# Kernel optimization log

Hardware: AMD Instinct MI355X
Metric: run time of the kernel (lower is better)

The kernel has to match this reference:

```python
import jax, jax.numpy as jnp
import numpy as np

B, IN_DIM, HID, ATT = 16384, 128, 512, 256
TOTAL = IN_DIM + HID + ATT


def setup_inputs() -> dict:
    key = jax.random.key(0)
    ks = jax.random.split(key, 10)
    u = lambda k, shape, lo, hi: jax.random.uniform(k, shape, jnp.float32, lo, hi)
    return {
        "t": jnp.float32(0.0),
        "h_ltc": jax.random.normal(ks[0], (B, HID), jnp.float32),
        "x_t": jax.random.normal(ks[1], (B, IN_DIM), jnp.float32),
        "context": jax.random.normal(ks[2], (B, ATT), jnp.float32),
        "W_gd": u(ks[3], (2 * HID, TOTAL), -0.1, 0.1),
        "b_gd": u(ks[4], (2 * HID,), -0.1, 0.1),
        "W_tau": u(ks[5], (HID, HID), -0.1, 0.1),
        "b_tau": u(ks[6], (HID,), -0.1, 0.1),
        "gleak": u(ks[7], (HID,), 0.001, 1.0),
        "cm": u(ks[8], (HID,), 0.4, 0.6),
    }


def reference(t, h_ltc, x_t, context, W_gd, b_gd, W_tau, b_tau, gleak, cm):
    # combined: [B, IN+HID+ATT]
    combined = jnp.concatenate([x_t, h_ltc, context], axis=1)
    g_d = combined @ W_gd.T + b_gd            # [B, 2*HID]
    gate, dynamics = jnp.split(g_d, 2, axis=1)
    tau = jax.nn.softplus(h_ltc @ W_tau.T + b_tau)  # [B, HID]
    numerator = jax.nn.sigmoid(gate) * jnp.tanh(dynamics) - h_ltc
    denominator = tau + jax.nn.softplus(cm) + jax.nn.softplus(gleak)
    return numerator / (denominator + 1e-6)
```

## Files before the change

kernel.cpp:

```cpp
#include <hip/hip_runtime.h>
#include <hip/hip_bf16.h>
#include <math.h>

#define BROWS 16384
#define IN_DIM 128
#define HID 512
#define ATT 256
#define KTOT 896
#define KC_TOT 112

typedef __bf16 bf16x8 __attribute__((ext_vector_type(8)));
typedef float f32x4 __attribute__((ext_vector_type(4)));

__device__ __forceinline__ float softplus_f(float x) {
    return fmaxf(x, 0.0f) + log1pf(__expf(-fabsf(x)));
}

__global__ void pack_B(const float* __restrict__ W_gd, const float* __restrict__ W_tau,
                       const float* __restrict__ gleak, const float* __restrict__ cm,
                       __hip_bfloat16* __restrict__ B_stage, float* __restrict__ dconst) {
    const int cid = blockIdx.x * 256 + threadIdx.x;
    if (cid < HID) {
        dconst[cid] = softplus_f(cm[cid]) + softplus_f(gleak[cid]) + 1e-6f;
    }
    const int nl = cid % 192;
    const int kc = (cid / 192) % KC_TOT;
    const int jt = cid / (192 * KC_TOT);
    const int jg = nl / 48, type = (nl % 48) / 16, j16 = nl % 16;
    const int j = jt * 64 + jg * 16 + j16;
    const int k0 = kc * 8;

    float v[8];
    if (type == 0) {
        const float* s = W_gd + (size_t)j * KTOT + k0;
        #pragma unroll
        for (int i = 0; i < 8; ++i) v[i] = s[i];
    } else if (type == 1) {
        const float* s = W_gd + (size_t)(HID + j) * KTOT + k0;
        #pragma unroll
        for (int i = 0; i < 8; ++i) v[i] = s[i];
    } else {
        if (k0 >= IN_DIM && k0 < IN_DIM + HID) {
            const float* s = W_tau + (size_t)j * HID + (k0 - IN_DIM);
            #pragma unroll
            for (int i = 0; i < 8; ++i) v[i] = s[i];
        } else {
            #pragma unroll
            for (int i = 0; i < 8; ++i) v[i] = 0.0f;
        }
    }
    union { __hip_bfloat16 hh[8]; uint4 u; } p;
    #pragma unroll
    for (int i = 0; i < 8; ++i) p.hh[i] = __float2bfloat16(v[i]);
    *(uint4*)(B_stage + (size_t)cid * 8) = p.u;
}

__device__ __forceinline__ void slab_src(int ks, const float* x, const float* h,
                                         const float* c, const float*& src,
                                         int& rs, int& c0) {
    if (ks < 2)       { src = x; rs = IN_DIM; c0 = ks * 64; }
    else if (ks < 10) { src = h; rs = HID;    c0 = (ks - 2) * 64; }
    else              { src = c; rs = ATT;    c0 = (ks - 10) * 64; }
}

__global__ __launch_bounds__(512, 4) void ltc_gemm(
    const float* __restrict__ x, const float* __restrict__ h_ltc,
    const float* __restrict__ ctx, const __hip_bfloat16* __restrict__ B_stage,
    const float* __restrict__ b_gd, const float* __restrict__ b_tau,
    const float* __restrict__ dconst, float* __restrict__ out) {

    __shared__ __attribute__((aligned(16))) char smem[16384 + 24576];
    char* As = smem;
    char* Bs = smem + 16384;

    const int bx = blockIdx.x;
    const int mt = bx & 127;
    const int jt = bx >> 7;
    const int tid = threadIdx.x;
    const int wave = tid >> 6, lane = tid & 63;
    const int wm = wave >> 2;
    const int wj = wave & 3;
    const int q = lane >> 4, t = lane & 15;

    const int kc8 = tid & 7;
    const int mi0 = tid >> 3;

    f32x4 accg[4], accd[4], acct[4];
    #pragma unroll
    for (int i = 0; i < 4; ++i) {
        accg[i] = (f32x4)0.0f; accd[i] = (f32x4)0.0f; acct[i] = (f32x4)0.0f;
    }

    const __hip_bfloat16* bSrc[3]; char* bDst[3];
    #pragma unroll
    for (int r = 0; r < 3; ++r) {
        int c = wave + 8 * r;
        bSrc[r] = B_stage + (size_t)jt * (KC_TOT * 1536) + c * 512 + lane * 8;
        bDst[r] = Bs + c * 1024;
    }

    float4 pf[2][2];
    {
        const float* src; int rs, c0;
        slab_src(0, x, h_ltc, ctx, src, rs, c0);
        #pragma unroll
        for (int r = 0; r < 2; ++r) {
            const float* p = src + (size_t)(mt * 128 + mi0 + 64 * r) * rs + c0 + kc8 * 8;
            pf[r][0] = *(const float4*)p;
            pf[r][1] = *(const float4*)(p + 4);
        }
    }

    for (int ks = 0; ks < 14; ++ks) {
        #pragma unroll
        for (int r = 0; r < 3; ++r)
            __builtin_amdgcn_global_load_lds(
                (const __attribute__((address_space(1))) void*)bSrc[r],
                (__attribute__((address_space(3))) void*)bDst[r], 16, 0, 0);
        #pragma unroll
        for (int r = 0; r < 2; ++r) {
            union { __hip_bfloat16 hh[8]; uint4 u; } pk;
            pk.hh[0] = __float2bfloat16(pf[r][0].x);
            pk.hh[1] = __float2bfloat16(pf[r][0].y);
            pk.hh[2] = __float2bfloat16(pf[r][0].z);
            pk.hh[3] = __float2bfloat16(pf[r][0].w);
            pk.hh[4] = __float2bfloat16(pf[r][1].x);
            pk.hh[5] = __float2bfloat16(pf[r][1].y);
            pk.hh[6] = __float2bfloat16(pf[r][1].z);
            pk.hh[7] = __float2bfloat16(pf[r][1].w);
            const int mi = mi0 + 64 * r;
            *(uint4*)(As + ((kc8 * 128 + (mi ^ kc8)) << 4)) = pk.u;
        }
        __syncthreads();

        if (ks < 13) {
            const float* src; int rs, c0;
            slab_src(ks + 1, x, h_ltc, ctx, src, rs, c0);
            #pragma unroll
            for (int r = 0; r < 2; ++r) {
                const float* p = src + (size_t)(mt * 128 + mi0 + 64 * r) * rs + c0 + kc8 * 8;
                pf[r][0] = *(const float4*)p;
                pf[r][1] = *(const float4*)(p + 4);
            }
        }

        const bool tau_on = (ks >= 2 && ks < 10);
        #pragma unroll
        for (int ko2 = 0; ko2 < 2; ++ko2) {
            const int kcl = ko2 * 4 + q;
            const char* ab = As + ((kcl * 128 + ((wm * 64 + t) ^ kcl)) << 4);
            bf16x8 a0 = *(const bf16x8*)(ab);
            bf16x8 a1 = *(const bf16x8*)(ab + 256);
            bf16x8 a2 = *(const bf16x8*)(ab + 512);
            bf16x8 a3 = *(const bf16x8*)(ab + 768);
            const char* bb = Bs + (((kcl * 192) + wj * 48 + t) << 4);
            bf16x8 bg = *(const bf16x8*)(bb);
            bf16x8 bd = *(const bf16x8*)(bb + 256);
            accg[0] = __builtin_amdgcn_mfma_f32_16x16x32_bf16(a0, bg, accg[0], 0, 0, 0);
            accg[1] = __builtin_amdgcn_mfma_f32_16x16x32_bf16(a1, bg, accg[1], 0, 0, 0);
            accg[2] = __builtin_amdgcn_mfma_f32_16x16x32_bf16(a2, bg, accg[2], 0, 0, 0);
            accg[3] = __builtin_amdgcn_mfma_f32_16x16x32_bf16(a3, bg, accg[3], 0, 0, 0);
            accd[0] = __builtin_amdgcn_mfma_f32_16x16x32_bf16(a0, bd, accd[0], 0, 0, 0);
            accd[1] = __builtin_amdgcn_mfma_f32_16x16x32_bf16(a1, bd, accd[1], 0, 0, 0);
            accd[2] = __builtin_amdgcn_mfma_f32_16x16x32_bf16(a2, bd, accd[2], 0, 0, 0);
            accd[3] = __builtin_amdgcn_mfma_f32_16x16x32_bf16(a3, bd, accd[3], 0, 0, 0);
            if (tau_on) {
                bf16x8 bt = *(const bf16x8*)(bb + 512);
                acct[0] = __builtin_amdgcn_mfma_f32_16x16x32_bf16(a0, bt, acct[0], 0, 0, 0);
                acct[1] = __builtin_amdgcn_mfma_f32_16x16x32_bf16(a1, bt, acct[1], 0, 0, 0);
                acct[2] = __builtin_amdgcn_mfma_f32_16x16x32_bf16(a2, bt, acct[2], 0, 0, 0);
                acct[3] = __builtin_amdgcn_mfma_f32_16x16x32_bf16(a3, bt, acct[3], 0, 0, 0);
            }
        }
        #pragma unroll
        for (int r = 0; r < 3; ++r) bSrc[r] += 12288;
        __syncthreads();
    }

    const int row0 = mt * 128 + wm * 64 + q * 4;
    const int j = jt * 64 + wj * 16 + t;
    const float bgj = b_gd[j];
    const float bdj = b_gd[HID + j];
    const float btj = b_tau[j];
    const float dcj = dconst[j];
    #pragma unroll
    for (int i = 0; i < 4; ++i) {
        #pragma unroll
        for (int r = 0; r < 4; ++r) {
            const int row = row0 + i * 16 + r;
            const float gv = accg[i][r] + bgj;
            const float dv = accd[i][r] + bdj;
            const float tp = acct[i][r] + btj;
            const float hv = h_ltc[(size_t)row * HID + j];
            const float sig = __builtin_amdgcn_rcpf(1.0f + __expf(-gv));
            const float th  = 1.0f - 2.0f * __builtin_amdgcn_rcpf(__expf(2.0f * dv) + 1.0f);
            const float tau = fmaxf(tp, 0.0f) + __logf(1.0f + __expf(-fabsf(tp)));
            out[(size_t)row * HID + j] = (sig * th - hv) * __builtin_amdgcn_rcpf(tau + dcj);
        }
    }
}

extern "C" void kernel_launch(void* const* d_in, const int* in_sizes, int n_in,
                              void* d_out, int out_size, void* d_ws, size_t ws_size,
                              hipStream_t stream) {
    const float* h_ltc = (const float*)d_in[1];
    const float* x_t   = (const float*)d_in[2];
    const float* ctx   = (const float*)d_in[3];
    const float* W_gd  = (const float*)d_in[4];
    const float* b_gd  = (const float*)d_in[5];
    const float* W_tau = (const float*)d_in[6];
    const float* b_tau = (const float*)d_in[7];
    const float* gleak = (const float*)d_in[8];
    const float* cm    = (const float*)d_in[9];

    char* ws = (char*)d_ws;
    __hip_bfloat16* B_stage = (__hip_bfloat16*)ws;
    float* dconst = (float*)(ws + 2752512);

    pack_B<<<672, 256, 0, stream>>>(W_gd, W_tau, gleak, cm, B_stage, dconst);
    ltc_gemm<<<1024, 512, 0, stream>>>(x_t, h_ltc, ctx, B_stage, b_gd, b_tau, dconst,
                                       (float*)d_out);
}
```

Baseline: 169.0 us.

## Halve output-column tile and double-buffer A/B LDS stages

Shrinks each block's output tile from 64 to 32 hidden columns, which doubles the grid to 2048 blocks. The eight waves are rearranged as a 4x2 grid, each holding a 32x16 sub-tile. A and B LDS buffers are now double-buffered with a two-deep register prefetch of activations, so the next slab's conversion and async B load overlap the current MFMA work and one barrier per step goes away. In exchange, activations are re-read from global memory twice as often and LDS use grows, which may lower occupancy.

Result: slower. 203.9 us (+20.6%).

```diff
diff --git a/kernel.cpp b/kernel.cpp
--- a/kernel.cpp
+++ b/kernel.cpp
@@ -23,11 +23,11 @@
     if (cid < HID) {
         dconst[cid] = softplus_f(cm[cid]) + softplus_f(gleak[cid]) + 1e-6f;
     }
-    const int nl = cid % 192;
-    const int kc = (cid / 192) % KC_TOT;
-    const int jt = cid / (192 * KC_TOT);
+    const int nl = cid % 96;
+    const int kc = (cid / 96) % KC_TOT;
+    const int jt = cid / (96 * KC_TOT);
     const int jg = nl / 48, type = (nl % 48) / 16, j16 = nl % 16;
-    const int j = jt * 64 + jg * 16 + j16;
+    const int j = jt * 32 + jg * 16 + j16;
     const int k0 = kc * 8;
 
     float v[8];
@@ -69,78 +69,121 @@
     const float* __restrict__ b_gd, const float* __restrict__ b_tau,
     const float* __restrict__ dconst, float* __restrict__ out) {
 
-    __shared__ __attribute__((aligned(16))) char smem[16384 + 24576];
-    char* As = smem;
-    char* Bs = smem + 16384;
+    __shared__ __attribute__((aligned(16))) char smem[2 * 16384 + 2 * 12288];
 
     const int bx = blockIdx.x;
     const int mt = bx & 127;
     const int jt = bx >> 7;
     const int tid = threadIdx.x;
     const int wave = tid >> 6, lane = tid & 63;
-    const int wm = wave >> 2;
-    const int wj = wave & 3;
+    const int wm = wave >> 1;
+    const int wj = wave & 1;
     const int q = lane >> 4, t = lane & 15;
 
     const int kc8 = tid & 7;
     const int mi0 = tid >> 3;
 
-    f32x4 accg[4], accd[4], acct[4];
+    f32x4 accg[2], accd[2], acct[2];
     #pragma unroll
-    for (int i = 0; i < 4; ++i) {
+    for (int i = 0; i < 2; ++i) {
         accg[i] = (f32x4)0.0f; accd[i] = (f32x4)0.0f; acct[i] = (f32x4)0.0f;
     }
 
-    const __hip_bfloat16* bSrc[3]; char* bDst[3];
-    #pragma unroll
-    for (int r = 0; r < 3; ++r) {
-        int c = wave + 8 * r;
-        bSrc[r] = B_stage + (size_t)jt * (KC_TOT * 1536) + c * 512 + lane * 8;
-        bDst[r] = Bs + c * 1024;
-    }
-
-    float4 pf[2][2];
+    const __hip_bfloat16* bSrc0 = B_stage + (size_t)jt * (KC_TOT * 768)
+                                + wave * 512 + lane * 8;
+    const __hip_bfloat16* bSrc1 = bSrc0 + 8 * 512;
+
+    float4 pf[2][2][2];
     {
         const float* src; int rs, c0;
         slab_src(0, x, h_ltc, ctx, src, rs, c0);
         #pragma unroll
         for (int r = 0; r < 2; ++r) {
             const float* p = src + (size_t)(mt * 128 + mi0 + 64 * r) * rs + c0 + kc8 * 8;
-            pf[r][0] = *(const float4*)p;
-            pf[r][1] = *(const float4*)(p + 4);
-        }
-    }
-
-    for (int ks = 0; ks < 14; ++ks) {
-        #pragma unroll
-        for (int r = 0; r < 3; ++r)
-            __builtin_amdgcn_global_load_lds(
-                (const __attribute__((address_space(1))) void*)bSrc[r],
-                (__attribute__((address_space(3))) void*)bDst[r], 16, 0, 0);
+            pf[0][r][0] = *(const float4*)p;
+            pf[0][r][1] = *(const float4*)(p + 4);
+        }
+    }
+    {
+        char* As0 = smem;
         #pragma unroll
         for (int r = 0; r < 2; ++r) {
             union { __hip_bfloat16 hh[8]; uint4 u; } pk;
-            pk.hh[0] = __float2bfloat16(pf[r][0].x);
-            pk.hh[1] = __float2bfloat16(pf[r][0].y);
-            pk.hh[2] = __float2bfloat16(pf[r][0].z);
-            pk.hh[3] = __float2bfloat16(pf[r][0].w);
-            pk.hh[4] = __float2bfloat16(pf[r][1].x);
-            pk.hh[5] = __float2bfloat16(pf[r][1].y);
-            pk.hh[6] = __float2bfloat16(pf[r][1].z);
-            pk.hh[7] = __float2bfloat16(pf[r][1].w);
+            pk.hh[0] = __float2bfloat16(pf[0][r][0].x);
+            pk.hh[1] = __float2bfloat16(pf[0][r][0].y);
+            pk.hh[2] = __float2bfloat16(pf[0][r][0].z);
+            pk.hh[3] = __float2bfloat16(pf[0][r][0].w);
+            pk.hh[4] = __float2bfloat16(pf[0][r][1].x);
+            pk.hh[5] = __float2bfloat16(pf[0][r][1].y);
+            pk.hh[6] = __float2bfloat16(pf[0][r][1].z);
+            pk.hh[7] = __float2bfloat16(pf[0][r][1].w);
             const int mi = mi0 + 64 * r;
-            *(uint4*)(As + ((kc8 * 128 + (mi ^ kc8)) << 4)) = pk.u;
-        }
-        __syncthreads();
+            *(uint4*)(As0 + ((kc8 * 128 + (mi ^ kc8)) << 4)) = pk.u;
+        }
+        char* Bs0 = smem + 32768;
+        __builtin_amdgcn_global_load_lds(
+            (const __attribute__((address_space(1))) void*)bSrc0,
+            (__attribute__((address_space(3))) void*)(Bs0 + wave * 1024), 16, 0, 0);
+        if (wave < 4)
+            __builtin_amdgcn_global_load_lds(
+                (const __attribute__((address_space(1))) void*)bSrc1,
+                (__attribute__((address_space(3))) void*)(Bs0 + (wave + 8) * 1024), 16, 0, 0);
+    }
+    {
+        const float* src; int rs, c0;
+        slab_src(1, x, h_ltc, ctx, src, rs, c0);
+        #pragma unroll
+        for (int r = 0; r < 2; ++r) {
+            const float* p = src + (size_t)(mt * 128 + mi0 + 64 * r) * rs + c0 + kc8 * 8;
+            pf[1][r][0] = *(const float4*)p;
+            pf[1][r][1] = *(const float4*)(p + 4);
+        }
+    }
+    __syncthreads();
+
+    for (int ks = 0; ks < 14; ++ks) {
+        const int cur = ks & 1, nxt = cur ^ 1;
+        char* AsC = smem + cur * 16384;
+        char* AsN = smem + nxt * 16384;
+        char* BsC = smem + 32768 + cur * 12288;
+        char* BsN = smem + 32768 + nxt * 12288;
 
         if (ks < 13) {
+            const int slot = (ks + 1) & 1;
+            #pragma unroll
+            for (int r = 0; r < 2; ++r) {
+                union { __hip_bfloat16 hh[8]; uint4 u; } pk;
+                pk.hh[0] = __float2bfloat16(pf[slot][r][0].x);
+                pk.hh[1] = __float2bfloat16(pf[slot][r][0].y);
+                pk.hh[2] = __float2bfloat16(pf[slot][r][0].z);
+                pk.hh[3] = __float2bfloat16(pf[slot][r][0].w);
+                pk.hh[4] = __float2bfloat16(pf[slot][r][1].x);
+                pk.hh[5] = __float2bfloat16(pf[slot][r][1].y);
+                pk.hh[6] = __float2bfloat16(pf[slot][r][1].z);
+                pk.hh[7] = __float2bfloat16(pf[slot][r][1].w);
+                const int mi = mi0 + 64 * r;
+                *(uint4*)(AsN + ((kc8 * 128 + (mi ^ kc8)) << 4)) = pk.u;
+            }
+            const __hip_bfloat16* b0 = bSrc0 + (size_t)(ks + 1) * 6144;
+            __builtin_amdgcn_global_load_lds(
+                (const __attribute__((address_space(1))) void*)b0,
+                (__attribute__((address_space(3))) void*)(BsN + wave * 1024), 16, 0, 0);
+            if (wave < 4) {
+                const __hip_bfloat16* b1 = bSrc1 + (size_t)(ks + 1) * 6144;
+                __builtin_amdgcn_global_load_lds(
+                    (const __attribute__((address_space(1))) void*)b1,
+                    (__attribute__((address_space(3))) void*)(BsN + (wave + 8) * 1024), 16, 0, 0);
+            }
+        }
+        if (ks < 12) {
             const float* src; int rs, c0;
-            slab_src(ks + 1, x, h_ltc, ctx, src, rs, c0);
+            slab_src(ks + 2, x, h_ltc, ctx, src, rs, c0);
+            const int slot = ks & 1;
             #pragma unroll
             for (int r = 0; r < 2; ++r) {
                 const float* p = src + (size_t)(mt * 128 + mi0 + 64 * r) * rs + c0 + kc8 * 8;
-                pf[r][0] = *(const float4*)p;
-                pf[r][1] = *(const float4*)(p + 4);
+                pf[slot][r][0] = *(const float4*)p;
+                pf[slot][r][1] = *(const float4*)(p + 4);
             }
         }
 
@@ -148,43 +191,33 @@
         #pragma unroll
         for (int ko2 = 0; ko2 < 2; ++ko2) {
             const int kcl = ko2 * 4 + q;
-            const char* ab = As + ((kcl * 128 + ((wm * 64 + t) ^ kcl)) << 4);
+            const char* ab = AsC + ((kcl * 128 + wm * 32 + (t ^ kcl)) << 4);
             bf16x8 a0 = *(const bf16x8*)(ab);
             bf16x8 a1 = *(const bf16x8*)(ab + 256);
-            bf16x8 a2 = *(const bf16x8*)(ab + 512);
-            bf16x8 a3 = *(const bf16x8*)(ab + 768);
-            const char* bb = Bs + (((kcl * 192) + wj * 48 + t) << 4);
+            const char* bb = BsC + ((kcl * 96 + wj * 48 + t) << 4);
             bf16x8 bg = *(const bf16x8*)(bb);
             bf16x8 bd = *(const bf16x8*)(bb + 256);
             accg[0] = __builtin_amdgcn_mfma_f32_16x16x32_bf16(a0, bg, accg[0], 0, 0, 0);
             accg[1] = __builtin_amdgcn_mfma_f32_16x16x32_bf16(a1, bg, accg[1], 0, 0, 0);
-            accg[2] = __builtin_amdgcn_mfma_f32_16x16x32_bf16(a2, bg, accg[2], 0, 0, 0);
-            accg[3] = __builtin_amdgcn_mfma_f32_16x16x32_bf16(a3, bg, accg[3], 0, 0, 0);
             accd[0] = __builtin_amdgcn_mfma_f32_16x16x32_bf16(a0, bd, accd[0], 0, 0, 0);
             accd[1] = __builtin_amdgcn_mfma_f32_16x16x32_bf16(a1, bd, accd[1], 0, 0, 0);
-            accd[2] = __builtin_amdgcn_mfma_f32_16x16x32_bf16(a2, bd, accd[2], 0, 0, 0);
-            accd[3] = __builtin_amdgcn_mfma_f32_16x16x32_bf16(a3, bd, accd[3], 0, 0, 0);
             if (tau_on) {
                 bf16x8 bt = *(const bf16x8*)(bb + 512);
                 acct[0] = __builtin_amdgcn_mfma_f32_16x16x32_bf16(a0, bt, acct[0], 0, 0, 0);
                 acct[1] = __builtin_amdgcn_mfma_f32_16x16x32_bf16(a1, bt, acct[1], 0, 0, 0);
-                acct[2] = __builtin_amdgcn_mfma_f32_16x16x32_bf16(a2, bt, acct[2], 0, 0, 0);
-                acct[3] = __builtin_amdgcn_mfma_f32_16x16x32_bf16(a3, bt, acct[3], 0, 0, 0);
-            }
-        }
-        #pragma unroll
-        for (int r = 0; r < 3; ++r) bSrc[r] += 12288;
+            }
+        }
         __syncthreads();
     }
 
-    const int row0 = mt * 128 + wm * 64 + q * 4;
-    const int j = jt * 64 + wj * 16 + t;
+    const int row0 = mt * 128 + wm * 32 + q * 4;
+    const int j = jt * 32 + wj * 16 + t;
     const float bgj = b_gd[j];
     const float bdj = b_gd[HID + j];
     const float btj = b_tau[j];
     const float dcj = dconst[j];
     #pragma unroll
-    for (int i = 0; i < 4; ++i) {
+    for (int i = 0; i < 2; ++i) {
         #pragma unroll
         for (int r = 0; r < 4; ++r) {
             const int row = row0 + i * 16 + r;
@@ -218,6 +251,6 @@
     float* dconst = (float*)(ws + 2752512);
 
     pack_B<<<672, 256, 0, stream>>>(W_gd, W_tau, gleak, cm, B_stage, dconst);
-    ltc_gemm<<<1024, 512, 0, stream>>>(x_t, h_ltc, ctx, B_stage, b_gd, b_tau, dconst,
+    ltc_gemm<<<2048, 512, 0, stream>>>(x_t, h_ltc, ctx, B_stage, b_gd, b_tau, dconst,
                                        (float*)d_out);
 }
```

## Double-buffer A tile in LDS and load B fragments directly from global

Applied to the files above, without the earlier changes.

Replaces the single A buffer plus LDS-staged B with a ping-pong A buffer in LDS, so the next slab is written while the current one is consumed and only one barrier per k-step remains. B fragments are now read by each wave straight from global memory into registers instead of going through global_load_lds. The A prefetch distance grows to two slabs and the loop is fully unrolled. This removes a barrier and the LDS staging traffic for B, but each wave now issues redundant global reads of B that rely on cache hits, and register pressure rises.

Result: no change. 171.9 us (+1.7%).

```diff
diff --git a/kernel.cpp b/kernel.cpp
--- a/kernel.cpp
+++ b/kernel.cpp
@@ -69,9 +69,7 @@
     const float* __restrict__ b_gd, const float* __restrict__ b_tau,
     const float* __restrict__ dconst, float* __restrict__ out) {
 
-    __shared__ __attribute__((aligned(16))) char smem[16384 + 24576];
-    char* As = smem;
-    char* Bs = smem + 16384;
+    __shared__ __attribute__((aligned(16))) char smem[2 * 16384];
 
     const int bx = blockIdx.x;
     const int mt = bx & 127;
@@ -91,13 +89,8 @@
         accg[i] = (f32x4)0.0f; accd[i] = (f32x4)0.0f; acct[i] = (f32x4)0.0f;
     }
 
-    const __hip_bfloat16* bSrc[3]; char* bDst[3];
-    #pragma unroll
-    for (int r = 0; r < 3; ++r) {
-        int c = wave + 8 * r;
-        bSrc[r] = B_stage + (size_t)jt * (KC_TOT * 1536) + c * 512 + lane * 8;
-        bDst[r] = Bs + c * 1024;
-    }
+    const __hip_bfloat16* bBase = B_stage + (size_t)jt * (KC_TOT * 1536)
+                                + (size_t)(wj * 48 + t) * 8;
 
     float4 pf[2][2];
     {
@@ -110,13 +103,8 @@
             pf[r][1] = *(const float4*)(p + 4);
         }
     }
-
-    for (int ks = 0; ks < 14; ++ks) {
-        #pragma unroll
-        for (int r = 0; r < 3; ++r)
-            __builtin_amdgcn_global_load_lds(
-                (const __attribute__((address_space(1))) void*)bSrc[r],
-                (__attribute__((address_space(3))) void*)bDst[r], 16, 0, 0);
+    {
+        char* As0 = smem;
         #pragma unroll
         for (int r = 0; r < 2; ++r) {
             union { __hip_bfloat16 hh[8]; uint4 u; } pk;
@@ -129,13 +117,56 @@
             pk.hh[6] = __float2bfloat16(pf[r][1].z);
             pk.hh[7] = __float2bfloat16(pf[r][1].w);
             const int mi = mi0 + 64 * r;
-            *(uint4*)(As + ((kc8 * 128 + (mi ^ kc8)) << 4)) = pk.u;
-        }
-        __syncthreads();
+            *(uint4*)(As0 + ((kc8 * 128 + (mi ^ kc8)) << 4)) = pk.u;
+        }
+    }
+    {
+        const float* src; int rs, c0;
+        slab_src(1, x, h_ltc, ctx, src, rs, c0);
+        #pragma unroll
+        for (int r = 0; r < 2; ++r) {
+            const float* p = src + (size_t)(mt * 128 + mi0 + 64 * r) * rs + c0 + kc8 * 8;
+            pf[r][0] = *(const float4*)p;
+            pf[r][1] = *(const float4*)(p + 4);
+        }
+    }
+    __syncthreads();
+
+    #pragma unroll
+    for (int ks = 0; ks < 14; ++ks) {
+        char* AsC = smem + (ks & 1) * 16384;
+        char* AsN = smem + ((ks & 1) ^ 1) * 16384;
+        const bool tau_on = (ks >= 2 && ks < 10);
+
+        bf16x8 Bv[2][3];
+        #pragma unroll
+        for (int ko2 = 0; ko2 < 2; ++ko2) {
+            const int kcl = ko2 * 4 + q;
+            const __hip_bfloat16* bp = bBase + (size_t)(ks * 8 + kcl) * 1536;
+            Bv[ko2][0] = *(const bf16x8*)(bp);
+            Bv[ko2][1] = *(const bf16x8*)(bp + 128);
+            if (tau_on) Bv[ko2][2] = *(const bf16x8*)(bp + 256);
+        }
 
         if (ks < 13) {
+            #pragma unroll
+            for (int r = 0; r < 2; ++r) {
+                union { __hip_bfloat16 hh[8]; uint4 u; } pk;
+                pk.hh[0] = __float2bfloat16(pf[r][0].x);
+                pk.hh[1] = __float2bfloat16(pf[r][0].y);
+                pk.hh[2] = __float2bfloat16(pf[r][0].z);
+                pk.hh[3] = __float2bfloat16(pf[r][0].w);
+                pk.hh[4] = __float2bfloat16(pf[r][1].x);
+                pk.hh[5] = __float2bfloat16(pf[r][1].y);
+                pk.hh[6] = __float2bfloat16(pf[r][1].z);
+                pk.hh[7] = __float2bfloat16(pf[r][1].w);
+                const int mi = mi0 + 64 * r;
+                *(uint4*)(AsN + ((kc8 * 128 + (mi ^ kc8)) << 4)) = pk.u;
+            }
+        }
+        if (ks < 12) {
             const float* src; int rs, c0;
-            slab_src(ks + 1, x, h_ltc, ctx, src, rs, c0);
+            slab_src(ks + 2, x, h_ltc, ctx, src, rs, c0);
             #pragma unroll
             for (int r = 0; r < 2; ++r) {
                 const float* p = src + (size_t)(mt * 128 + mi0 + 64 * r) * rs + c0 + kc8 * 8;
@@ -144,36 +175,29 @@
             }
         }
 
-        const bool tau_on = (ks >= 2 && ks < 10);
         #pragma unroll
         for (int ko2 = 0; ko2 < 2; ++ko2) {
             const int kcl = ko2 * 4 + q;
-            const char* ab = As + ((kcl * 128 + ((wm * 64 + t) ^ kcl)) << 4);
+            const char* ab = AsC + ((kcl * 128 + ((wm * 64 + t) ^ kcl)) << 4);
             bf16x8 a0 = *(const bf16x8*)(ab);
             bf16x8 a1 = *(const bf16x8*)(ab + 256);
             bf16x8 a2 = *(const bf16x8*)(ab + 512);
             bf16x8 a3 = *(const bf16x8*)(ab + 768);
-            const char* bb = Bs + (((kcl * 192) + wj * 48 + t) << 4);
-            bf16x8 bg = *(const bf16x8*)(bb);
-            bf16x8 bd = *(const bf16x8*)(bb + 256);
-            accg[0] = __builtin_amdgcn_mfma_f32_16x16x32_bf16(a0, bg, accg[0], 0, 0, 0);
-            accg[1] = __builtin_amdgcn_mfma_f32_16x16x32_bf16(a1, bg, accg[1], 0, 0, 0);
-            accg[2] = __builtin_amdgcn_mfma_f32_16x16x32_bf16(a2, bg, accg[2], 0, 0, 0);
-            accg[3] = __builtin_amdgcn_mfma_f32_16x16x32_bf16(a3, bg, accg[3], 0, 0, 0);
-            accd[0] = __builtin_amdgcn_mfma_f32_16x16x32_bf16(a0, bd, accd[0], 0, 0, 0);
-            accd[1] = __builtin_amdgcn_mfma_f32_16x16x32_bf16(a1, bd, accd[1], 0, 0, 0);
-            accd[2] = __builtin_amdgcn_mfma_f32_16x16x32_bf16(a2, bd, accd[2], 0, 0, 0);
-            accd[3] = __builtin_amdgcn_mfma_f32_16x16x32_bf16(a3, bd, accd[3], 0, 0, 0);
+            accg[0] = __builtin_amdgcn_mfma_f32_16x16x32_bf16(a0, Bv[ko2][0], accg[0], 0, 0, 0);
+            accg[1] = __builtin_amdgcn_mfma_f32_16x16x32_bf16(a1, Bv[ko2][0], accg[1], 0, 0, 0);
+            accg[2] = __builtin_amdgcn_mfma_f32_16x16x32_bf16(a2, Bv[ko2][0], accg[2], 0, 0, 0);
+            accg[3] = __builtin_amdgcn_mfma_f32_16x16x32_bf16(a3, Bv[ko2][0], accg[3], 0, 0, 0);
+            accd[0] = __builtin_amdgcn_mfma_f32_16x16x32_bf16(a0, Bv[ko2][1], accd[0], 0, 0, 0);
+            accd[1] = __builtin_amdgcn_mfma_f32_16x16x32_bf16(a1, Bv[ko2][1], accd[1], 0, 0, 0);
+            accd[2] = __builtin_amdgcn_mfma_f32_16x16x32_bf16(a2, Bv[ko2][1], accd[2], 0, 0, 0);
+            accd[3] = __builtin_amdgcn_mfma_f32_16x16x32_bf16(a3, Bv[ko2][1], accd[3], 0, 0, 0);
             if (tau_on) {
-                bf16x8 bt = *(const bf16x8*)(bb + 512);
-                acct[0] = __builtin_amdgcn_mfma_f32_16x16x32_bf16(a0, bt, acct[0], 0, 0, 0);
-                acct[1] = __builtin_amdgcn_mfma_f32_16x16x32_bf16(a1, bt, acct[1], 0, 0, 0);
-                acct[2] = __builtin_amdgcn_mfma_f32_16x16x32_bf16(a2, bt, acct[2], 0, 0, 0);
-                acct[3] = __builtin_amdgcn_mfma_f32_16x16x32_bf16(a3, bt, acct[3], 0, 0, 0);
+                acct[0] = __builtin_amdgcn_mfma_f32_16x16x32_bf16(a0, Bv[ko2][2], acct[0], 0, 0, 0);
+                acct[1] = __builtin_amdgcn_mfma_f32_16x16x32_bf16(a1, Bv[ko2][2], acct[1], 0, 0, 0);
+                acct[2] = __builtin_amdgcn_mfma_f32_16x16x32_bf16(a2, Bv[ko2][2], acct[2], 0, 0, 0);
+                acct[3] = __builtin_amdgcn_mfma_f32_16x16x32_bf16(a3, Bv[ko2][2], acct[3], 0, 0, 0);
             }
         }
-        #pragma unroll
-        for (int r = 0; r < 3; ++r) bSrc[r] += 12288;
         __syncthreads();
     }
 
```

## Keep full-K A tile of 32 rows in LDS and stream B from global

Applied to the files above, without the earlier changes.

Each block now converts a 32-row slab of the concatenated input (all 896 K columns) to bf16 once into 56KB of LDS, then loops over all 512 output columns in four passes. B fragments are read directly from global/L2 into registers with software double-buffering, which removes the per-K-step barriers and LDS staging of B. The activation input is read and converted only once instead of eight times across column tiles. In exchange, B traffic shifts to per-wave global loads with no LDS reuse, and the 56KB LDS footprint lowers occupancy.

Result: faster. 165.7 us (-2.0%).

```diff
diff --git a/kernel.cpp b/kernel.cpp
--- a/kernel.cpp
+++ b/kernel.cpp
@@ -55,147 +55,108 @@
     *(uint4*)(B_stage + (size_t)cid * 8) = p.u;
 }
 
-__device__ __forceinline__ void slab_src(int ks, const float* x, const float* h,
-                                         const float* c, const float*& src,
-                                         int& rs, int& c0) {
-    if (ks < 2)       { src = x; rs = IN_DIM; c0 = ks * 64; }
-    else if (ks < 10) { src = h; rs = HID;    c0 = (ks - 2) * 64; }
-    else              { src = c; rs = ATT;    c0 = (ks - 10) * 64; }
-}
-
 __global__ __launch_bounds__(512, 4) void ltc_gemm(
     const float* __restrict__ x, const float* __restrict__ h_ltc,
     const float* __restrict__ ctx, const __hip_bfloat16* __restrict__ B_stage,
     const float* __restrict__ b_gd, const float* __restrict__ b_tau,
     const float* __restrict__ dconst, float* __restrict__ out) {
 
-    __shared__ __attribute__((aligned(16))) char smem[16384 + 24576];
-    char* As = smem;
-    char* Bs = smem + 16384;
+    __shared__ __attribute__((aligned(16))) char As[57344];
 
-    const int bx = blockIdx.x;
-    const int mt = bx & 127;
-    const int jt = bx >> 7;
+    const int mt = blockIdx.x;
     const int tid = threadIdx.x;
     const int wave = tid >> 6, lane = tid & 63;
-    const int wm = wave >> 2;
-    const int wj = wave & 3;
     const int q = lane >> 4, t = lane & 15;
 
-    const int kc8 = tid & 7;
-    const int mi0 = tid >> 3;
+    const int mi = tid >> 4;
+    const int kcg = tid & 15;
+    #pragma unroll
+    for (int s = 0; s < 7; ++s) {
+        const int kc = kcg + 16 * s;
+        const float* src; int rs, col;
+        if (s == 0)      { src = x;     rs = IN_DIM; col = kcg * 8; }
+        else if (s < 5)  { src = h_ltc; rs = HID;    col = kcg * 8 + (s - 1) * 128; }
+        else             { src = ctx;   rs = ATT;    col = kcg * 8 + (s - 5) * 128; }
+        const float* p = src + (size_t)(mt * 32 + mi) * rs + col;
+        float4 v0 = *(const float4*)p;
+        float4 v1 = *(const float4*)(p + 4);
+        union { __hip_bfloat16 hh[8]; uint4 u; } pk;
+        pk.hh[0] = __float2bfloat16(v0.x); pk.hh[1] = __float2bfloat16(v0.y);
+        pk.hh[2] = __float2bfloat16(v0.z); pk.hh[3] = __float2bfloat16(v0.w);
+        pk.hh[4] = __float2bfloat16(v1.x); pk.hh[5] = __float2bfloat16(v1.y);
+        pk.hh[6] = __float2bfloat16(v1.z); pk.hh[7] = __float2bfloat16(v1.w);
+        *(uint4*)(As + ((kc * 32 + (mi ^ (kc & 31))) << 4)) = pk.u;
+    }
+    __syncthreads();
 
-    f32x4 accg[4], accd[4], acct[4];
-    #pragma unroll
-    for (int i = 0; i < 4; ++i) {
-        accg[i] = (f32x4)0.0f; accd[i] = (f32x4)0.0f; acct[i] = (f32x4)0.0f;
-    }
+    for (int it = 0; it < 4; ++it) {
+        const int jglob = it * 128 + wave * 16;
+        const int jt = jglob >> 6;
+        const int jg = (jglob >> 4) & 3;
+        const __hip_bfloat16* bBase = B_stage
+            + ((size_t)jt * (KC_TOT * 192) + jg * 48 + t) * 8;
 
-    const __hip_bfloat16* bSrc[3]; char* bDst[3];
-    #pragma unroll
-    for (int r = 0; r < 3; ++r) {
-        int c = wave + 8 * r;
-        bSrc[r] = B_stage + (size_t)jt * (KC_TOT * 1536) + c * 512 + lane * 8;
-        bDst[r] = Bs + c * 1024;
-    }
+        f32x4 acc[2][3];
+        #pragma unroll
+        for (int f = 0; f < 2; ++f)
+            #pragma unroll
+            for (int ty = 0; ty < 3; ++ty) acc[f][ty] = (f32x4)0.0f;
 
-    float4 pf[2][2];
-    {
-        const float* src; int rs, c0;
-        slab_src(0, x, h_ltc, ctx, src, rs, c0);
-        #pragma unroll
-        for (int r = 0; r < 2; ++r) {
-            const float* p = src + (size_t)(mt * 128 + mi0 + 64 * r) * rs + c0 + kc8 * 8;
-            pf[r][0] = *(const float4*)p;
-            pf[r][1] = *(const float4*)(p + 4);
+        bf16x8 ab[2][2]; bf16x8 bb[2][3];
+
+        {
+            const int kc = q;
+            ab[0][0] = *(const bf16x8*)(As + ((kc * 32 + (t ^ kc)) << 4));
+            ab[0][1] = *(const bf16x8*)(As + ((kc * 32 + ((16 + t) ^ kc)) << 4));
+            const __hip_bfloat16* bp = bBase + (size_t)kc * 1536;
+            bb[0][0] = *(const bf16x8*)(bp);
+            bb[0][1] = *(const bf16x8*)(bp + 128);
         }
-    }
 
-    for (int ks = 0; ks < 14; ++ks) {
-        #pragma unroll
-        for (int r = 0; r < 3; ++r)
-            __builtin_amdgcn_global_load_lds(
-                (const __attribute__((address_space(1))) void*)bSrc[r],
-                (__attribute__((address_space(3))) void*)bDst[r], 16, 0, 0);
-        #pragma unroll
-        for (int r = 0; r < 2; ++r) {
-            union { __hip_bfloat16 hh[8]; uint4 u; } pk;
-            pk.hh[0] = __float2bfloat16(pf[r][0].x);
-            pk.hh[1] = __float2bfloat16(pf[r][0].y);
-            pk.hh[2] = __float2bfloat16(pf[r][0].z);
-            pk.hh[3] = __float2bfloat16(pf[r][0].w);
-            pk.hh[4] = __float2bfloat16(pf[r][1].x);
-            pk.hh[5] = __float2bfloat16(pf[r][1].y);
-            pk.hh[6] = __float2bfloat16(pf[r][1].z);
-            pk.hh[7] = __float2bfloat16(pf[r][1].w);
-            const int mi = mi0 + 64 * r;
-            *(uint4*)(As + ((kc8 * 128 + (mi ^ kc8)) << 4)) = pk.u;
-        }
-        __syncthreads();
-
-        if (ks < 13) {
-            const float* src; int rs, c0;
-            slab_src(ks + 1, x, h_ltc, ctx, src, rs, c0);
-            #pragma unroll
-            for (int r = 0; r < 2; ++r) {
-                const float* p = src + (size_t)(mt * 128 + mi0 + 64 * r) * rs + c0 + kc8 * 8;
-                pf[r][0] = *(const float4*)p;
-                pf[r][1] = *(const float4*)(p + 4);
+        #pragma unroll 4
+        for (int kst = 0; kst < 28; ++kst) {
+            const int cb = kst & 1, nb = cb ^ 1;
+            const bool tau_cur = (kst >= 4 && kst < 20);
+            if (kst < 27) {
+                const int kc = (kst + 1) * 4 + q;
+                const int sw = kc & 31;
+                ab[nb][0] = *(const bf16x8*)(As + ((kc * 32 + (t ^ sw)) << 4));
+                ab[nb][1] = *(const bf16x8*)(As + ((kc * 32 + ((16 + t) ^ sw)) << 4));
+                const __hip_bfloat16* bp = bBase + (size_t)kc * 1536;
+                bb[nb][0] = *(const bf16x8*)(bp);
+                bb[nb][1] = *(const bf16x8*)(bp + 128);
+                if (kst + 1 >= 4 && kst + 1 < 20)
+                    bb[nb][2] = *(const bf16x8*)(bp + 256);
+            }
+            acc[0][0] = __builtin_amdgcn_mfma_f32_16x16x32_bf16(ab[cb][0], bb[cb][0], acc[0][0], 0, 0, 0);
+            acc[1][0] = __builtin_amdgcn_mfma_f32_16x16x32_bf16(ab[cb][1], bb[cb][0], acc[1][0], 0, 0, 0);
+            acc[0][1] = __builtin_amdgcn_mfma_f32_16x16x32_bf16(ab[cb][0], bb[cb][1], acc[0][1], 0, 0, 0);
+            acc[1][1] = __builtin_amdgcn_mfma_f32_16x16x32_bf16(ab[cb][1], bb[cb][1], acc[1][1], 0, 0, 0);
+            if (tau_cur) {
+                acc[0][2] = __builtin_amdgcn_mfma_f32_16x16x32_bf16(ab[cb][0], bb[cb][2], acc[0][2], 0, 0, 0);
+                acc[1][2] = __builtin_amdgcn_mfma_f32_16x16x32_bf16(ab[cb][1], bb[cb][2], acc[1][2], 0, 0, 0);
             }
         }
 
-        const bool tau_on = (ks >= 2 && ks < 10);
+        const int j = jglob + t;
+        const float bgj = b_gd[j];
+        const float bdj = b_gd[HID + j];
+        const float btj = b_tau[j];
+        const float dcj = dconst[j];
         #pragma unroll
-        for (int ko2 = 0; ko2 < 2; ++ko2) {
-            const int kcl = ko2 * 4 + q;
-            const char* ab = As + ((kcl * 128 + ((wm * 64 + t) ^ kcl)) << 4);
-            bf16x8 a0 = *(const bf16x8*)(ab);
-            bf16x8 a1 = *(const bf16x8*)(ab + 256);
-            bf16x8 a2 = *(const bf16x8*)(ab + 512);
-            bf16x8 a3 = *(const bf16x8*)(ab + 768);
-            const char* bb = Bs + (((kcl * 192) + wj * 48 + t) << 4);
-            bf16x8 bg = *(const bf16x8*)(bb);
-            bf16x8 bd = *(const bf16x8*)(bb + 256);
-            accg[0] = __builtin_amdgcn_mfma_f32_16x16x32_bf16(a0, bg, accg[0], 0, 0, 0);
-            accg[1] = __builtin_amdgcn_mfma_f32_16x16x32_bf16(a1, bg, accg[1], 0, 0, 0);
-            accg[2] = __builtin_amdgcn_mfma_f32_16x16x32_bf16(a2, bg, accg[2], 0, 0, 0);
-            accg[3] = __builtin_amdgcn_mfma_f32_16x16x32_bf16(a3, bg, accg[3], 0, 0, 0);
-            accd[0] = __builtin_amdgcn_mfma_f32_16x16x32_bf16(a0, bd, accd[0], 0, 0, 0);
-            accd[1] = __builtin_amdgcn_mfma_f32_16x16x32_bf16(a1, bd, accd[1], 0, 0, 0);
-            accd[2] = __builtin_amdgcn_mfma_f32_16x16x32_bf16(a2, bd, accd[2], 0, 0, 0);
-            accd[3] = __builtin_amdgcn_mfma_f32_16x16x32_bf16(a3, bd, accd[3], 0, 0, 0);
-            if (tau_on) {
-                bf16x8 bt = *(const bf16x8*)(bb + 512);
-                acct[0] = __builtin_amdgcn_mfma_f32_16x16x32_bf16(a0, bt, acct[0], 0, 0, 0);
-                acct[1] = __builtin_amdgcn_mfma_f32_16x16x32_bf16(a1, bt, acct[1], 0, 0, 0);
-                acct[2] = __builtin_amdgcn_mfma_f32_16x16x32_bf16(a2, bt, acct[2], 0, 0, 0);
-                acct[3] = __builtin_amdgcn_mfma_f32_16x16x32_bf16(a3, bt, acct[3], 0, 0, 0);
+        for (int f = 0; f < 2; ++f) {
+            #pragma unroll
+            for (int r = 0; r < 4; ++r) {
+                const int row = mt * 32 + f * 16 + q * 4 + r;
+                const float gv = acc[f][0][r] + bgj;
+                const float dv = acc[f][1][r] + bdj;
+                const float tp = acc[f][2][r] + btj;
+                const float hv = h_ltc[(size_t)row * HID + j];
+                const float sig = __builtin_amdgcn_rcpf(1.0f + __expf(-gv));
+                const float th  = 1.0f - 2.0f * __builtin_amdgcn_rcpf(__expf(2.0f * dv) + 1.0f);
+                const float tau = fmaxf(tp, 0.0f) + __logf(1.0f + __expf(-fabsf(tp)));
+                out[(size_t)row * HID + j] = (sig * th - hv) * __builtin_amdgcn_rcpf(tau + dcj);
             }
-        }
-        #pragma unroll
-        for (int r = 0; r < 3; ++r) bSrc[r] += 12288;
-        __syncthreads();
-    }
-
-    const int row0 = mt * 128 + wm * 64 + q * 4;
-    const int j = jt * 64 + wj * 16 + t;
-    const float bgj = b_gd[j];
-    const float bdj = b_gd[HID + j];
-    const float btj = b_tau[j];
-    const float dcj = dconst[j];
-    #pragma unroll
-    for (int i = 0; i < 4; ++i) {
-        #pragma unroll
-        for (int r = 0; r < 4; ++r) {
-            const int row = row0 + i * 16 + r;
-            const float gv = accg[i][r] + bgj;
-            const float dv = accd[i][r] + bdj;
-            const float tp = acct[i][r] + btj;
-            const float hv = h_ltc[(size_t)row * HID + j];
-            const float sig = __builtin_amdgcn_rcpf(1.0f + __expf(-gv));
-            const float th  = 1.0f - 2.0f * __builtin_amdgcn_rcpf(__expf(2.0f * dv) + 1.0f);
-            const float tau = fmaxf(tp, 0.0f) + __logf(1.0f + __expf(-fabsf(tp)));
-            out[(size_t)row * HID + j] = (sig * th - hv) * __builtin_amdgcn_rcpf(tau + dcj);
         }
     }
 }
@@ -218,6 +179,6 @@
     float* dconst = (float*)(ws + 2752512);
 
     pack_B<<<672, 256, 0, stream>>>(W_gd, W_tau, gleak, cm, B_stage, dconst);
-    ltc_gemm<<<1024, 512, 0, stream>>>(x_t, h_ltc, ctx, B_stage, b_gd, b_tau, dconst,
-                                       (float*)d_out);
+    ltc_gemm<<<512, 512, 0, stream>>>(x_t, h_ltc, ctx, B_stage, b_gd, b_tau, dconst,
+                                      (float*)d_out);
 }
```
